# Kernel tuning notes

Measured on AMD Instinct MI355X. Metric: run time of the kernel, lower is better.

The kernel has to match this reference:

```python
import jax, jax.numpy as jnp
import numpy as np

SLOT_DIM, EMB_DIM, HID, ACT_DIM, NUM_ACT = 256, 256, 1024, 128, 1024
EPS_SAMPLE = 1e-6
EPS_LN = 1e-5


def setup_inputs() -> dict:
    key = jax.random.key(0)
    ks = jax.random.split(key, 12)
    B, N, S = 128, 32, 12
    s = 0.02
    return {
        "slots": jax.random.normal(ks[0], (B, N, S, SLOT_DIM), jnp.float32),
        "noise": jax.random.normal(ks[1], (B, N - 1, S, ACT_DIM), jnp.float32),
        "W1": jax.random.normal(ks[2], (SLOT_DIM, HID), jnp.float32) * s,
        "b1": jnp.zeros((HID,), jnp.float32),
        "ln_g": jnp.ones((HID,), jnp.float32),
        "ln_b": jnp.zeros((HID,), jnp.float32),
        "W2": jax.random.normal(ks[3], (HID, EMB_DIM), jnp.float32) * s,
        "b2": jnp.zeros((EMB_DIM,), jnp.float32),
        "Wm": jax.random.normal(ks[4], (EMB_DIM, ACT_DIM), jnp.float32) * s,
        "bm": jnp.zeros((ACT_DIM,), jnp.float32),
        "Wv": jax.random.normal(ks[5], (EMB_DIM, ACT_DIM), jnp.float32) * s,
        "bv": jnp.zeros((ACT_DIM,), jnp.float32),
        "codebook": jax.random.normal(ks[6], (NUM_ACT, ACT_DIM), jnp.float32) * s,
    }


def reference(slots, noise, W1, b1, ln_g, ln_b, W2, b2, Wm, bm, Wv, bv, codebook):
    sg = jax.lax.stop_gradient
    B, N, S, _ = slots.shape
    # per-slot MLP encoder: Linear -> ReLU -> LayerNorm -> Linear
    h = jax.nn.relu(jnp.einsum('bnsd,dh->bnsh', slots, W1) + b1)
    mu = h.mean(-1, keepdims=True)
    var = h.var(-1, keepdims=True)
    h = (h - mu) * jax.lax.rsqrt(var + EPS_LN) * ln_g + ln_b
    e = jnp.einsum('bnsh,he->bnse', h, W2) + b2  # (B,N,S,emb)
    # action distribution from consecutive frames
    mean_tok = jnp.einsum('bnse,ea->bnsa', e, Wm) + bm
    var_tok = jnp.abs(jnp.einsum('bnse,ea->bnsa', e, Wv) + bv)
    adm = mean_tok[:, 1:] - mean_tok[:, :-1]  # (B,N-1,S,A)
    adv = var_tok[:, 1:] + var_tok[:, :-1]
    action_dist = jnp.stack([adm, adv], axis=2)  # (B,N-1,2,S,A)
    # reparameterized sample
    z = noise * jnp.sqrt(adv + EPS_SAMPLE) + adm
    # VQ: nearest codebook entry via squared L2 distances
    zf = z.reshape(-1, ACT_DIM)  # (M,A)
    d = (jnp.sum(zf * zf, axis=1, keepdims=True)
         - 2.0 * zf @ codebook.T
         + jnp.sum(codebook * codebook, axis=1))  # (M,num_actions)
    idx = jnp.argmin(d, axis=1)  # (M,)
    q = codebook[idx].reshape(z.shape)
    quant_loss = jnp.mean((sg(z) - q) ** 2)
    commit_loss = jnp.mean((z - sg(q)) ** 2)
    q_st = z + sg(q - z)  # straight-through action prototypes
    action_variability = z - sg(q)
    action_idxs = idx.reshape(B, N - 1, S, 1)
    return (action_dist, z, action_variability, q_st, action_idxs, quant_loss, commit_loss)
```

## Files before the change

### kernel.cpp

```cpp
#include <hip/hip_runtime.h>
#include <math.h>

#define R_ROWS 49152
#define HID 1024
#define SLOT 256
#define EMB 256
#define ACT 128
#define NCODE 1024
#define M_ROWS 47616

#define OFF_AD 0
#define OFF_Z  12189696
#define OFF_AV 18284544
#define OFF_QS 24379392
#define OFF_IDX 30474240
#define OFF_QL 30521856
#define OFF_CL 30521857

#define WS_MT    0
#define WS_VT    6291456
#define WS_W1H  12582912
#define WS_W1L  12713984
#define WS_W2H  12845056
#define WS_W2L  12976128
#define WS_WMH  13107200
#define WS_WML  13123584
#define WS_WVH  13139968
#define WS_WVL  13156352
#define WS_CBH  13172736
#define WS_CBL  13238272
#define WS_CN   13303808
#define WS_LOSS 13304832

typedef _Float16 f16x8 __attribute__((ext_vector_type(8)));
typedef float f32x4 __attribute__((ext_vector_type(4)));
typedef float f32x16 __attribute__((ext_vector_type(16)));

__device__ __forceinline__ void pack_body(
    const float* __restrict__ W, _Float16* __restrict__ hi, _Float16* __restrict__ lo,
    int lgS, int N, int p)
{
    int j = p & 7;
    int l = (p >> 3) & 63;
    int q = p >> 9;
    int s = q & ((1 << lgS) - 1);
    int t = q >> lgS;
    int n = t * 16 + (l & 15);
    int k = s * 32 + ((l >> 4) << 3) + j;
    float x = W[(size_t)k * N + n];
    _Float16 h = (_Float16)x;
    hi[p] = h;
    lo[p] = (_Float16)(x - (float)h);
}

__global__ __launch_bounds__(256) void k_packall(
    const float* __restrict__ W1, const float* __restrict__ W2,
    const float* __restrict__ Wm, const float* __restrict__ Wv,
    const float* __restrict__ CB,
    _Float16* __restrict__ W1h, _Float16* __restrict__ W1l,
    _Float16* __restrict__ W2h, _Float16* __restrict__ W2l,
    _Float16* __restrict__ Wmh, _Float16* __restrict__ Wml,
    _Float16* __restrict__ Wvh, _Float16* __restrict__ Wvl,
    _Float16* __restrict__ CBh, _Float16* __restrict__ CBl,
    float* __restrict__ cn, float* __restrict__ losss)
{
    const int bi = blockIdx.x;
    const int tid = threadIdx.x;
    if (bi == 0 && tid == 0) *losss = 0.f;

    if (bi < 1024) {
        pack_body(W1, W1h, W1l, 3, HID, bi * 256 + tid);
    } else if (bi < 2048) {
        pack_body(W2, W2h, W2l, 5, EMB, (bi - 1024) * 256 + tid);
    } else if (bi < 2176) {
        pack_body(Wm, Wmh, Wml, 3, ACT, (bi - 2048) * 256 + tid);
    } else if (bi < 2304) {
        pack_body(Wv, Wvh, Wvl, 3, ACT, (bi - 2176) * 256 + tid);
    } else if (bi < 2816) {
        int p = (bi - 2304) * 256 + tid;
        int j = p & 7;
        int l = (p >> 3) & 63;
        int q = p >> 9;
        int s = q & 7;
        int t = q >> 3;
        int n = t * 32 + (l & 31);
        int k = s * 16 + ((l >> 5) << 3) + j;
        float x = CB[(size_t)n * ACT + k];
        _Float16 h = (_Float16)x;
        CBh[p] = h;
        CBl[p] = (_Float16)(x - (float)h);
    } else {
        int c = (bi - 2816) * 256 + tid;
        float s = 0.f;
        #pragma unroll
        for (int k = 0; k < ACT; k += 4) {
            float4 v = *(const float4*)&CB[(size_t)c * ACT + k];
            s += v.x*v.x + v.y*v.y + v.z*v.z + v.w*v.w;
        }
        cn[c] = s;
    }
}

__global__ __launch_bounds__(512, 4) void k_encoder_mfma(
    const float* __restrict__ X,
    const float* __restrict__ b1, const float* __restrict__ ln_g, const float* __restrict__ ln_b,
    const float* __restrict__ b2, const float* __restrict__ bm, const float* __restrict__ bv,
    const _Float16* __restrict__ W1h, const _Float16* __restrict__ W1l,
    const _Float16* __restrict__ W2h, const _Float16* __restrict__ W2l,
    const _Float16* __restrict__ Wmh, const _Float16* __restrict__ Wml,
    const _Float16* __restrict__ Wvh, const _Float16* __restrict__ Wvl,
    float* __restrict__ MT, float* __restrict__ VT)
{
    __shared__ _Float16 Hh0[16][1024];
    __shared__ _Float16 Hh1[16][1024];

    const int tid = threadIdx.x;
    const int w  = tid >> 6;
    const int l  = tid & 63;
    const int lr = l & 15;
    const int lg = l >> 4;
    const long rowbase = (long)blockIdx.x * 16;

    f16x8 a0[8], a1[8];
    {
        const float* xrow = X + (rowbase + lr) * SLOT + lg * 8;
        #pragma unroll
        for (int s = 0; s < 8; ++s) {
            float4 xa = *(const float4*)(xrow + 32 * s);
            float4 xb = *(const float4*)(xrow + 32 * s + 4);
            float xv[8] = {xa.x, xa.y, xa.z, xa.w, xb.x, xb.y, xb.z, xb.w};
            #pragma unroll
            for (int e = 0; e < 8; ++e) {
                _Float16 h = (_Float16)xv[e];
                a0[s][e] = h;
                a1[s][e] = (_Float16)(xv[e] - (float)h);
            }
        }
    }

    f32x4 acc[8];
    #pragma unroll
    for (int t = 0; t < 8; ++t) acc[t] = (f32x4){0.f, 0.f, 0.f, 0.f};

    #pragma unroll
    for (int s = 0; s < 8; ++s) {
        #pragma unroll
        for (int t = 0; t < 8; ++t) {
            int tg = w * 8 + t;
            f16x8 bh = *(const f16x8*)(W1h + ((size_t)(tg * 8 + s) * 64 + l) * 8);
            f16x8 bl = *(const f16x8*)(W1l + ((size_t)(tg * 8 + s) * 64 + l) * 8);
            acc[t] = __builtin_amdgcn_mfma_f32_16x16x32_f16(a0[s], bh, acc[t], 0, 0, 0);
            acc[t] = __builtin_amdgcn_mfma_f32_16x16x32_f16(a0[s], bl, acc[t], 0, 0, 0);
            acc[t] = __builtin_amdgcn_mfma_f32_16x16x32_f16(a1[s], bh, acc[t], 0, 0, 0);
        }
    }

    #pragma unroll
    for (int t = 0; t < 8; ++t) {
        float bb = b1[w * 128 + t * 16 + lr];
        #pragma unroll
        for (int r = 0; r < 4; ++r) acc[t][r] = fmaxf(acc[t][r] + bb, 0.f);
    }

    float sum[4] = {0,0,0,0}, sq[4] = {0,0,0,0};
    #pragma unroll
    for (int t = 0; t < 8; ++t)
        #pragma unroll
        for (int r = 0; r < 4; ++r) {
            float v = acc[t][r];
            sum[r] += v; sq[r] = fmaf(v, v, sq[r]);
        }
    #pragma unroll
    for (int off = 1; off < 16; off <<= 1)
        #pragma unroll
        for (int r = 0; r < 4; ++r) {
            sum[r] += __shfl_xor(sum[r], off, 64);
            sq[r]  += __shfl_xor(sq[r],  off, 64);
        }
    float* stat = (float*)&Hh0[0][0];
    if (lr == 0) {
        #pragma unroll
        for (int r = 0; r < 4; ++r) {
            stat[w * 16 + 4 * lg + r]       = sum[r];
            stat[128 + w * 16 + 4 * lg + r] = sq[r];
        }
    }
    __syncthreads();
    float mu[4], rs[4];
    #pragma unroll
    for (int r = 0; r < 4; ++r) {
        int m = 4 * lg + r;
        float s = 0.f, q = 0.f;
        #pragma unroll
        for (int wv = 0; wv < 8; ++wv) {
            s += stat[wv * 16 + m];
            q += stat[128 + wv * 16 + m];
        }
        float mmu = s * (1.f / HID);
        float var = q * (1.f / HID) - mmu * mmu;
        mu[r] = mmu;
        rs[r] = 1.f / sqrtf(var + 1e-5f);
    }
    __syncthreads();

    #pragma unroll
    for (int t = 0; t < 8; ++t) {
        int n = w * 128 + t * 16 + lr;
        float g = ln_g[n], be = ln_b[n];
        #pragma unroll
        for (int r = 0; r < 4; ++r) {
            int m = 4 * lg + r;
            float v = (acc[t][r] - mu[r]) * rs[r] * g + be;
            _Float16 h = (_Float16)v;
            _Float16 lo = (_Float16)(v - (float)h);
            int c = n >> 3, jj = n & 7;
            int cs = c ^ (m & 7);
            Hh0[m][cs * 8 + jj] = h;
            Hh1[m][cs * 8 + jj] = lo;
        }
    }
    __syncthreads();

    f32x4 acc2[2];
    #pragma unroll
    for (int t = 0; t < 2; ++t) acc2[t] = (f32x4){0.f, 0.f, 0.f, 0.f};

    #pragma unroll 4
    for (int s = 0; s < 32; ++s) {
        int cs = (4 * s + lg) ^ (lr & 7);
        f16x8 ah = *(const f16x8*)&Hh0[lr][cs * 8];
        f16x8 al = *(const f16x8*)&Hh1[lr][cs * 8];
        #pragma unroll
        for (int t = 0; t < 2; ++t) {
            int tg = w * 2 + t;
            f16x8 bh = *(const f16x8*)(W2h + ((size_t)(tg * 32 + s) * 64 + l) * 8);
            f16x8 bl = *(const f16x8*)(W2l + ((size_t)(tg * 32 + s) * 64 + l) * 8);
            acc2[t] = __builtin_amdgcn_mfma_f32_16x16x32_f16(ah, bh, acc2[t], 0, 0, 0);
            acc2[t] = __builtin_amdgcn_mfma_f32_16x16x32_f16(ah, bl, acc2[t], 0, 0, 0);
            acc2[t] = __builtin_amdgcn_mfma_f32_16x16x32_f16(al, bh, acc2[t], 0, 0, 0);
        }
    }
    __syncthreads();

    _Float16* Es0 = &Hh0[0][0];
    _Float16* Es1 = &Hh0[0][0] + 4096;
    #pragma unroll
    for (int t = 0; t < 2; ++t) {
        int n = w * 32 + t * 16 + lr;
        float bb2 = b2[n];
        #pragma unroll
        for (int r = 0; r < 4; ++r) {
            int m = 4 * lg + r;
            float v = acc2[t][r] + bb2;
            _Float16 h = (_Float16)v;
            _Float16 lo = (_Float16)(v - (float)h);
            int c = n >> 3, jj = n & 7;
            int cs = c ^ (m & 7);
            Es0[m * 256 + cs * 8 + jj] = h;
            Es1[m * 256 + cs * 8 + jj] = lo;
        }
    }
    __syncthreads();

    const _Float16* WXh = (w < 4) ? Wmh : Wvh;
    const _Float16* WXl = (w < 4) ? Wml : Wvl;
    f32x4 acc3[2];
    #pragma unroll
    for (int t = 0; t < 2; ++t) acc3[t] = (f32x4){0.f, 0.f, 0.f, 0.f};

    #pragma unroll
    for (int s = 0; s < 8; ++s) {
        int cs = (4 * s + lg) ^ (lr & 7);
        f16x8 ah = *(const f16x8*)&Es0[lr * 256 + cs * 8];
        f16x8 al = *(const f16x8*)&Es1[lr * 256 + cs * 8];
        #pragma unroll
        for (int t = 0; t < 2; ++t) {
            int tg = (w & 3) * 2 + t;
            f16x8 bh = *(const f16x8*)(WXh + ((size_t)(tg * 8 + s) * 64 + l) * 8);
            f16x8 bl = *(const f16x8*)(WXl + ((size_t)(tg * 8 + s) * 64 + l) * 8);
            acc3[t] = __builtin_amdgcn_mfma_f32_16x16x32_f16(ah, bh, acc3[t], 0, 0, 0);
            acc3[t] = __builtin_amdgcn_mfma_f32_16x16x32_f16(ah, bl, acc3[t], 0, 0, 0);
            acc3[t] = __builtin_amdgcn_mfma_f32_16x16x32_f16(al, bh, acc3[t], 0, 0, 0);
        }
    }

    #pragma unroll
    for (int t = 0; t < 2; ++t) {
        int a = (w & 3) * 32 + t * 16 + lr;
        float bx = (w < 4) ? bm[a] : bv[a];
        #pragma unroll
        for (int r = 0; r < 4; ++r) {
            float v = acc3[t][r] + bx;
            size_t row = rowbase + 4 * lg + r;
            if (w < 4) MT[row * ACT + a] = v;
            else       VT[row * ACT + a] = fabsf(v);
        }
    }
}

__global__ __launch_bounds__(256, 2) void k_vqfused(
    const float* __restrict__ MT, const float* __restrict__ VT,
    const float* __restrict__ noise,
    const _Float16* __restrict__ CBh, const _Float16* __restrict__ CBl,
    const float* __restrict__ cn, const float* __restrict__ CB,
    float* __restrict__ out, float* __restrict__ losss)
{
    __shared__ float4 Zs4[4096];
    __shared__ int   idx_s[128];
    __shared__ float red[4];
    float* Zs = (float*)Zs4;

    const int tid = threadIdx.x;
    const int rowbase = blockIdx.x * 128;
    const int a = tid & 127;
    const int rhalf = tid >> 7;

    #pragma unroll 8
    for (int i = 0; i < 64; ++i) {
        int row = 2 * i + rhalf;
        int m = rowbase + row;
        int b = m / 372;
        int r1 = m + 12 * b;
        int r2 = r1 + 12;
        float m1 = MT[(size_t)r1 * ACT + a], m2 = MT[(size_t)r2 * ACT + a];
        float v1 = VT[(size_t)r1 * ACT + a], v2 = VT[(size_t)r2 * ACT + a];
        float adm = m2 - m1;
        float adv = v2 + v1;
        float z = noise[(size_t)m * ACT + a] * sqrtf(adv + 1e-6f) + adm;
        int np = m / 12, s = m - np * 12;
        out[OFF_AD + (size_t)(np * 24 + s) * ACT + a] = adm;
        out[OFF_AD + (size_t)(np * 24 + 12 + s) * ACT + a] = adv;
        out[OFF_Z + (size_t)m * ACT + a] = z;
        Zs[row * 128 + (((a >> 2) ^ (row & 31)) << 2) + (a & 3)] = z;
    }
    __syncthreads();

    const int w = tid >> 6, l = tid & 63;
    const int col = l & 31, hw = l >> 5;
    const int arow = 32 * w + col;

    f16x8 a0[8], a1[8];
    #pragma unroll
    for (int s = 0; s < 8; ++s) {
        #pragma unroll
        for (int half = 0; half < 2; ++half) {
            int k4 = s * 4 + hw * 2 + half;
            float4 v = *(const float4*)&Zs[arow * 128 + ((k4 ^ (arow & 31)) << 2)];
            float xv[4] = {v.x, v.y, v.z, v.w};
            #pragma unroll
            for (int e = 0; e < 4; ++e) {
                _Float16 h = (_Float16)xv[e];
                a0[s][half * 4 + e] = h;
                a1[s][half * 4 + e] = (_Float16)(xv[e] - (float)h);
            }
        }
    }

    float best[16];
    int bidx[16];
    #pragma unroll
    for (int r = 0; r < 16; ++r) { best[r] = 3.4e38f; bidx[r] = 0; }

    for (int cb = 0; cb < 4; ++cb) {
        f32x16 acc[8];
        #pragma unroll
        for (int t = 0; t < 8; ++t)
            #pragma unroll
            for (int r = 0; r < 16; ++r) acc[t][r] = 0.f;

        #pragma unroll
        for (int s = 0; s < 8; ++s) {
            #pragma unroll
            for (int t = 0; t < 8; ++t) {
                int tg = cb * 8 + t;
                f16x8 bh = *(const f16x8*)(CBh + ((size_t)(tg * 8 + s) * 64 + l) * 8);
                f16x8 bl = *(const f16x8*)(CBl + ((size_t)(tg * 8 + s) * 64 + l) * 8);
                acc[t] = __builtin_amdgcn_mfma_f32_32x32x16_f16(a0[s], bh, acc[t], 0, 0, 0);
                acc[t] = __builtin_amdgcn_mfma_f32_32x32x16_f16(a0[s], bl, acc[t], 0, 0, 0);
                acc[t] = __builtin_amdgcn_mfma_f32_32x32x16_f16(a1[s], bh, acc[t], 0, 0, 0);
            }
        }

        float cnv[8];
        #pragma unroll
        for (int t = 0; t < 8; ++t) cnv[t] = cn[cb * 256 + t * 32 + col];

        #pragma unroll
        for (int reg = 0; reg < 16; ++reg) {
            #pragma unroll
            for (int t = 0; t < 8; ++t) {
                float d = cnv[t] - 2.f * acc[t][reg];
                int gi = cb * 256 + t * 32 + col;
                if (d < best[reg]) { best[reg] = d; bidx[reg] = gi; }
            }
        }
    }

    #pragma unroll
    for (int reg = 0; reg < 16; ++reg) {
        float bv_ = best[reg];
        int bi_ = bidx[reg];
        #pragma unroll
        for (int off = 1; off < 32; off <<= 1) {
            float ov = __shfl_xor(bv_, off, 64);
            int   oi = __shfl_xor(bi_, off, 64);
            if (ov < bv_ || (ov == bv_ && oi < bi_)) { bv_ = ov; bi_ = oi; }
        }
        if (col == 0) {
            int mloc = 32 * w + (reg & 3) + 8 * (reg >> 2) + 4 * hw;
            idx_s[mloc] = bi_;
            out[OFF_IDX + rowbase + mloc] = (float)bi_;
        }
    }
    __syncthreads();

    float ls = 0.f;
    #pragma unroll 8
    for (int i = 0; i < 64; ++i) {
        int row = 2 * i + rhalf;
        float z = Zs[row * 128 + (((a >> 2) ^ (row & 31)) << 2) + (a & 3)];
        int ci = idx_s[row];
        float q = CB[(size_t)ci * ACT + a];
        float diff = z - q;
        size_t m = (size_t)(rowbase + row);
        out[OFF_QS + m * ACT + a] = z + (q - z);
        out[OFF_AV + m * ACT + a] = diff;
        ls = fmaf(diff, diff, ls);
    }
    #pragma unroll
    for (int off = 32; off; off >>= 1) ls += __shfl_xor(ls, off, 64);
    if (l == 0) red[w] = ls;
    __syncthreads();
    if (tid == 0) atomicAdd(losss, red[0] + red[1] + red[2] + red[3]);
}

__global__ void k_losses(const float* __restrict__ losss, float* __restrict__ out)
{
    float v = *losss * (1.f / 6094848.f);
    out[OFF_QL] = v;
    out[OFF_CL] = v;
}

extern "C" void kernel_launch(void* const* d_in, const int* in_sizes, int n_in,
                              void* d_out, int out_size, void* d_ws, size_t ws_size,
                              hipStream_t stream)
{
    const float* slots = (const float*)d_in[0];
    const float* noise = (const float*)d_in[1];
    const float* W1    = (const float*)d_in[2];
    const float* b1    = (const float*)d_in[3];
    const float* ln_g  = (const float*)d_in[4];
    const float* ln_b  = (const float*)d_in[5];
    const float* W2    = (const float*)d_in[6];
    const float* b2    = (const float*)d_in[7];
    const float* Wm    = (const float*)d_in[8];
    const float* bm    = (const float*)d_in[9];
    const float* Wv    = (const float*)d_in[10];
    const float* bv    = (const float*)d_in[11];
    const float* CB    = (const float*)d_in[12];
    float* out = (float*)d_out;
    float* ws  = (float*)d_ws;

    float* MT   = ws + WS_MT;
    float* VT   = ws + WS_VT;
    float* cn   = ws + WS_CN;
    float* losss = ws + WS_LOSS;

    _Float16* W1h = (_Float16*)(ws + WS_W1H);
    _Float16* W1l = (_Float16*)(ws + WS_W1L);
    _Float16* W2h = (_Float16*)(ws + WS_W2H);
    _Float16* W2l = (_Float16*)(ws + WS_W2L);
    _Float16* Wmh = (_Float16*)(ws + WS_WMH);
    _Float16* Wml = (_Float16*)(ws + WS_WML);
    _Float16* Wvh = (_Float16*)(ws + WS_WVH);
    _Float16* Wvl = (_Float16*)(ws + WS_WVL);
    _Float16* CBh = (_Float16*)(ws + WS_CBH);
    _Float16* CBl = (_Float16*)(ws + WS_CBL);

    hipLaunchKernelGGL(k_packall, dim3(2820), dim3(256), 0, stream,
                       W1, W2, Wm, Wv, CB,
                       W1h, W1l, W2h, W2l, Wmh, Wml, Wvh, Wvl, CBh, CBl, cn, losss);
    hipLaunchKernelGGL(k_encoder_mfma, dim3(R_ROWS/16), dim3(512), 0, stream,
                       slots, b1, ln_g, ln_b, b2, bm, bv,
                       W1h, W1l, W2h, W2l, Wmh, Wml, Wvh, Wvl, MT, VT);
    hipLaunchKernelGGL(k_vqfused, dim3(M_ROWS/128), dim3(256), 0, stream,
                       MT, VT, noise, CBh, CBl, cn, CB, out, losss);
    hipLaunchKernelGGL(k_losses, dim3(1), dim3(1), 0, stream, losss, out);
}
```

Before: 447.4 us.

## Split encoder into tiled GEMM1/GEMM2 kernels with folded LayerNorm affine

Replaces the single fused encoder kernel, in which each 16-row block reloaded all of W1 and W2 from global memory, with two kernels. The first stages a 64-column slice of W1 in LDS and computes 128 rows per block, writing ReLU activations as fp16 hi/lo pairs plus per-slice LayerNorm partial sums to workspace. The second tiles 64 rows per block for the W2 and Wm/Wv GEMMs, and applies LayerNorm after the matmul by folding ln_g into W2 and precomputing ln_b·W2 + b2 and ln_g·W2 vectors. Rows are processed in two chunks so the intermediate buffer fits. This improves weight reuse but adds a global round trip for the hidden activations and more kernel launches, and the post-matmul normalisation may change rounding behaviour.

```diff
diff --git a/kernel.cpp b/kernel.cpp
--- a/kernel.cpp
+++ b/kernel.cpp
@@ -1,13 +1,14 @@
 #include <hip/hip_runtime.h>
 #include <math.h>
 
-#define R_ROWS 49152
 #define HID 1024
 #define SLOT 256
 #define EMB 256
 #define ACT 128
 #define NCODE 1024
+#define R_ROWS 49152
 #define M_ROWS 47616
+#define CH_ROWS 24576
 
 #define OFF_AD 0
 #define OFF_Z  12189696
@@ -30,15 +31,19 @@
 #define WS_CBH  13172736
 #define WS_CBL  13238272
 #define WS_CN   13303808
-#define WS_LOSS 13304832
+#define WS_V0   13304832
+#define WS_V1   13305088
+#define WS_LOSS 13305344
+#define WS_STATS 13305600
+#define WS_HH   14092032
+#define WS_HL   26674944
 
 typedef _Float16 f16x8 __attribute__((ext_vector_type(8)));
 typedef float f32x4 __attribute__((ext_vector_type(4)));
-typedef float f32x16 __attribute__((ext_vector_type(16)));
 
 __device__ __forceinline__ void pack_body(
     const float* __restrict__ W, _Float16* __restrict__ hi, _Float16* __restrict__ lo,
-    int lgS, int N, int p)
+    int lgS, int N, int p, const float* __restrict__ scale)
 {
     int j = p & 7;
     int l = (p >> 3) & 63;
@@ -48,6 +53,7 @@
     int n = t * 16 + (l & 15);
     int k = s * 32 + ((l >> 4) << 3) + j;
     float x = W[(size_t)k * N + n];
+    if (scale) x *= scale[k];
     _Float16 h = (_Float16)x;
     hi[p] = h;
     lo[p] = (_Float16)(x - (float)h);
@@ -56,26 +62,28 @@
 __global__ __launch_bounds__(256) void k_packall(
     const float* __restrict__ W1, const float* __restrict__ W2,
     const float* __restrict__ Wm, const float* __restrict__ Wv,
-    const float* __restrict__ CB,
+    const float* __restrict__ CB, const float* __restrict__ ln_g,
+    const float* __restrict__ ln_b, const float* __restrict__ b2,
     _Float16* __restrict__ W1h, _Float16* __restrict__ W1l,
     _Float16* __restrict__ W2h, _Float16* __restrict__ W2l,
     _Float16* __restrict__ Wmh, _Float16* __restrict__ Wml,
     _Float16* __restrict__ Wvh, _Float16* __restrict__ Wvl,
     _Float16* __restrict__ CBh, _Float16* __restrict__ CBl,
-    float* __restrict__ cn, float* __restrict__ losss)
+    float* __restrict__ cn, float* __restrict__ v0, float* __restrict__ v1,
+    float* __restrict__ losss)
 {
     const int bi = blockIdx.x;
     const int tid = threadIdx.x;
     if (bi == 0 && tid == 0) *losss = 0.f;
 
     if (bi < 1024) {
-        pack_body(W1, W1h, W1l, 3, HID, bi * 256 + tid);
+        pack_body(W1, W1h, W1l, 3, HID, bi * 256 + tid, (const float*)0);
     } else if (bi < 2048) {
-        pack_body(W2, W2h, W2l, 5, EMB, (bi - 1024) * 256 + tid);
+        pack_body(W2, W2h, W2l, 5, EMB, (bi - 1024) * 256 + tid, ln_g);
     } else if (bi < 2176) {
-        pack_body(Wm, Wmh, Wml, 3, ACT, (bi - 2048) * 256 + tid);
+        pack_body(Wm, Wmh, Wml, 3, ACT, (bi - 2048) * 256 + tid, (const float*)0);
     } else if (bi < 2304) {
-        pack_body(Wv, Wvh, Wvl, 3, ACT, (bi - 2176) * 256 + tid);
+        pack_body(Wv, Wvh, Wvl, 3, ACT, (bi - 2176) * 256 + tid, (const float*)0);
     } else if (bi < 2816) {
         int p = (bi - 2304) * 256 + tid;
         int j = p & 7;
@@ -89,7 +97,7 @@
         _Float16 h = (_Float16)x;
         CBh[p] = h;
         CBl[p] = (_Float16)(x - (float)h);
-    } else {
+    } else if (bi < 2820) {
         int c = (bi - 2816) * 256 + tid;
         float s = 0.f;
         #pragma unroll
@@ -98,32 +106,47 @@
             s += v.x*v.x + v.y*v.y + v.z*v.z + v.w*v.w;
         }
         cn[c] = s;
+    } else {
+        int n = tid;
+        float a0 = 0.f, a1 = 0.f;
+        for (int c = 0; c < HID; ++c) {
+            float w2 = W2[(size_t)c * EMB + n];
+            a1 = fmaf(ln_g[c], w2, a1);
+            a0 = fmaf(ln_b[c], w2, a0);
+        }
+        v1[n] = a1;
+        v0[n] = a0 + b2[n];
     }
 }
 
-__global__ __launch_bounds__(512, 4) void k_encoder_mfma(
-    const float* __restrict__ X,
-    const float* __restrict__ b1, const float* __restrict__ ln_g, const float* __restrict__ ln_b,
-    const float* __restrict__ b2, const float* __restrict__ bm, const float* __restrict__ bv,
+__global__ __launch_bounds__(512, 4) void k_gemm1(
+    const float* __restrict__ X, const float* __restrict__ b1,
     const _Float16* __restrict__ W1h, const _Float16* __restrict__ W1l,
-    const _Float16* __restrict__ W2h, const _Float16* __restrict__ W2l,
-    const _Float16* __restrict__ Wmh, const _Float16* __restrict__ Wml,
-    const _Float16* __restrict__ Wvh, const _Float16* __restrict__ Wvl,
-    float* __restrict__ MT, float* __restrict__ VT)
+    _Float16* __restrict__ GHh, _Float16* __restrict__ GHl,
+    float* __restrict__ stats, int row0)
 {
-    __shared__ _Float16 Hh0[16][1024];
-    __shared__ _Float16 Hh1[16][1024];
+    __shared__ _Float16 sh[32768];
 
     const int tid = threadIdx.x;
-    const int w  = tid >> 6;
-    const int l  = tid & 63;
-    const int lr = l & 15;
-    const int lg = l >> 4;
-    const long rowbase = (long)blockIdx.x * 16;
+    const int w = tid >> 6, l = tid & 63, lr = l & 15, lg = l >> 4;
+    const int p = blockIdx.x & 15;
+    const int rg = blockIdx.x >> 4;
+    const int rowc = rg * 128;
+
+    {
+        const float4* s0 = (const float4*)(W1h + (size_t)p * 16384);
+        const float4* s1 = (const float4*)(W1l + (size_t)p * 16384);
+        float4* d = (float4*)sh;
+        #pragma unroll
+        for (int i = 0; i < 4; ++i) {
+            d[tid + 512 * i] = s0[tid + 512 * i];
+            d[2048 + tid + 512 * i] = s1[tid + 512 * i];
+        }
+    }
 
     f16x8 a0[8], a1[8];
     {
-        const float* xrow = X + (rowbase + lr) * SLOT + lg * 8;
+        const float* xrow = X + (size_t)(row0 + rowc + w * 16 + lr) * SLOT + lg * 8;
         #pragma unroll
         for (int s = 0; s < 8; ++s) {
             float4 xa = *(const float4*)(xrow + 32 * s);
@@ -137,18 +160,18 @@
             }
         }
     }
-
-    f32x4 acc[8];
-    #pragma unroll
-    for (int t = 0; t < 8; ++t) acc[t] = (f32x4){0.f, 0.f, 0.f, 0.f};
+    __syncthreads();
+
+    f32x4 acc[4];
+    #pragma unroll
+    for (int t = 0; t < 4; ++t) acc[t] = (f32x4){0.f, 0.f, 0.f, 0.f};
 
     #pragma unroll
     for (int s = 0; s < 8; ++s) {
         #pragma unroll
-        for (int t = 0; t < 8; ++t) {
-            int tg = w * 8 + t;
-            f16x8 bh = *(const f16x8*)(W1h + ((size_t)(tg * 8 + s) * 64 + l) * 8);
-            f16x8 bl = *(const f16x8*)(W1l + ((size_t)(tg * 8 + s) * 64 + l) * 8);
+        for (int t = 0; t < 4; ++t) {
+            f16x8 bh = *(const f16x8*)&sh[((t * 8 + s) * 64 + l) * 8];
+            f16x8 bl = *(const f16x8*)&sh[16384 + ((t * 8 + s) * 64 + l) * 8];
             acc[t] = __builtin_amdgcn_mfma_f32_16x16x32_f16(a0[s], bh, acc[t], 0, 0, 0);
             acc[t] = __builtin_amdgcn_mfma_f32_16x16x32_f16(a0[s], bl, acc[t], 0, 0, 0);
             acc[t] = __builtin_amdgcn_mfma_f32_16x16x32_f16(a1[s], bh, acc[t], 0, 0, 0);
@@ -156,144 +179,225 @@
     }
 
     #pragma unroll
-    for (int t = 0; t < 8; ++t) {
-        float bb = b1[w * 128 + t * 16 + lr];
+    for (int t = 0; t < 4; ++t) {
+        float bb = b1[p * 64 + t * 16 + lr];
         #pragma unroll
         for (int r = 0; r < 4; ++r) acc[t][r] = fmaxf(acc[t][r] + bb, 0.f);
     }
 
-    float sum[4] = {0,0,0,0}, sq[4] = {0,0,0,0};
-    #pragma unroll
-    for (int t = 0; t < 8; ++t)
+    {
+        float sum[4] = {0,0,0,0}, sq[4] = {0,0,0,0};
+        #pragma unroll
+        for (int t = 0; t < 4; ++t)
+            #pragma unroll
+            for (int r = 0; r < 4; ++r) {
+                float v = acc[t][r];
+                sum[r] += v; sq[r] = fmaf(v, v, sq[r]);
+            }
+        #pragma unroll
+        for (int off = 1; off < 16; off <<= 1)
+            #pragma unroll
+            for (int r = 0; r < 4; ++r) {
+                sum[r] += __shfl_xor(sum[r], off, 64);
+                sq[r]  += __shfl_xor(sq[r],  off, 64);
+            }
+        if (lr == 0) {
+            #pragma unroll
+            for (int r = 0; r < 4; ++r) {
+                size_t row = (size_t)rowc + w * 16 + lg * 4 + r;
+                float2 st = {sum[r], sq[r]};
+                *(float2*)&stats[((size_t)p * CH_ROWS + row) * 2] = st;
+            }
+        }
+    }
+    __syncthreads();
+
+    #pragma unroll
+    for (int t = 0; t < 4; ++t) {
         #pragma unroll
         for (int r = 0; r < 4; ++r) {
+            int rowloc = w * 16 + lg * 4 + r;
+            int col = t * 16 + lr;
+            int cc = col >> 3, j = col & 7;
+            int ad = rowloc * 64 + ((cc ^ (rowloc & 7)) << 3) + j;
             float v = acc[t][r];
-            sum[r] += v; sq[r] = fmaf(v, v, sq[r]);
-        }
-    #pragma unroll
-    for (int off = 1; off < 16; off <<= 1)
-        #pragma unroll
-        for (int r = 0; r < 4; ++r) {
-            sum[r] += __shfl_xor(sum[r], off, 64);
-            sq[r]  += __shfl_xor(sq[r],  off, 64);
-        }
-    float* stat = (float*)&Hh0[0][0];
-    if (lr == 0) {
-        #pragma unroll
-        for (int r = 0; r < 4; ++r) {
-            stat[w * 16 + 4 * lg + r]       = sum[r];
-            stat[128 + w * 16 + 4 * lg + r] = sq[r];
-        }
-    }
-    __syncthreads();
-    float mu[4], rs[4];
-    #pragma unroll
-    for (int r = 0; r < 4; ++r) {
-        int m = 4 * lg + r;
+            _Float16 h = (_Float16)v;
+            sh[ad] = h;
+            sh[8192 + ad] = (_Float16)(v - (float)h);
+        }
+    }
+    __syncthreads();
+
+    #pragma unroll
+    for (int i = 0; i < 2; ++i) {
+        int u = tid + 512 * i;
+        int RTl = u >> 7;
+        int Sl  = (u >> 6) & 1;
+        int li  = u & 63;
+        int row = RTl * 16 + (li & 15);
+        int cc  = Sl * 4 + (li >> 4);
+        int ad  = row * 64 + ((cc ^ (row & 7)) << 3);
+        f16x8 vh = *(const f16x8*)&sh[ad];
+        f16x8 vl = *(const f16x8*)&sh[8192 + ad];
+        size_t RTg = (size_t)rg * 8 + RTl;
+        size_t off = ((RTg * 32 + (2 * p + Sl)) * 64 + li) * 8;
+        *(f16x8*)&GHh[off] = vh;
+        *(f16x8*)&GHl[off] = vl;
+    }
+}
+
+__global__ __launch_bounds__(512, 4) void k_gemm2(
+    const _Float16* __restrict__ GHh, const _Float16* __restrict__ GHl,
+    const _Float16* __restrict__ W2h, const _Float16* __restrict__ W2l,
+    const _Float16* __restrict__ Wmh, const _Float16* __restrict__ Wml,
+    const _Float16* __restrict__ Wvh, const _Float16* __restrict__ Wvl,
+    const float* __restrict__ stats, const float* __restrict__ v0,
+    const float* __restrict__ v1, const float* __restrict__ bm,
+    const float* __restrict__ bv,
+    float* __restrict__ MT, float* __restrict__ VT, int row0)
+{
+    __shared__ _Float16 sh[32768];
+    __shared__ float mu_s[64], rs_s[64];
+
+    const int tid = threadIdx.x;
+    const int w = tid >> 6, l = tid & 63, lr = l & 15, lg = l >> 4;
+    const int rb = blockIdx.x;
+    const int rowc0 = rb * 64;
+
+    if (tid < 64) {
         float s = 0.f, q = 0.f;
         #pragma unroll
-        for (int wv = 0; wv < 8; ++wv) {
-            s += stat[wv * 16 + m];
-            q += stat[128 + wv * 16 + m];
-        }
-        float mmu = s * (1.f / HID);
-        float var = q * (1.f / HID) - mmu * mmu;
-        mu[r] = mmu;
-        rs[r] = 1.f / sqrtf(var + 1e-5f);
-    }
-    __syncthreads();
-
-    #pragma unroll
-    for (int t = 0; t < 8; ++t) {
-        int n = w * 128 + t * 16 + lr;
-        float g = ln_g[n], be = ln_b[n];
-        #pragma unroll
-        for (int r = 0; r < 4; ++r) {
-            int m = 4 * lg + r;
-            float v = (acc[t][r] - mu[r]) * rs[r] * g + be;
-            _Float16 h = (_Float16)v;
-            _Float16 lo = (_Float16)(v - (float)h);
-            int c = n >> 3, jj = n & 7;
-            int cs = c ^ (m & 7);
-            Hh0[m][cs * 8 + jj] = h;
-            Hh1[m][cs * 8 + jj] = lo;
-        }
-    }
-    __syncthreads();
-
-    f32x4 acc2[2];
-    #pragma unroll
-    for (int t = 0; t < 2; ++t) acc2[t] = (f32x4){0.f, 0.f, 0.f, 0.f};
-
-    #pragma unroll 4
-    for (int s = 0; s < 32; ++s) {
-        int cs = (4 * s + lg) ^ (lr & 7);
-        f16x8 ah = *(const f16x8*)&Hh0[lr][cs * 8];
-        f16x8 al = *(const f16x8*)&Hh1[lr][cs * 8];
-        #pragma unroll
-        for (int t = 0; t < 2; ++t) {
-            int tg = w * 2 + t;
-            f16x8 bh = *(const f16x8*)(W2h + ((size_t)(tg * 32 + s) * 64 + l) * 8);
-            f16x8 bl = *(const f16x8*)(W2l + ((size_t)(tg * 32 + s) * 64 + l) * 8);
-            acc2[t] = __builtin_amdgcn_mfma_f32_16x16x32_f16(ah, bh, acc2[t], 0, 0, 0);
-            acc2[t] = __builtin_amdgcn_mfma_f32_16x16x32_f16(ah, bl, acc2[t], 0, 0, 0);
-            acc2[t] = __builtin_amdgcn_mfma_f32_16x16x32_f16(al, bh, acc2[t], 0, 0, 0);
-        }
-    }
-    __syncthreads();
-
-    _Float16* Es0 = &Hh0[0][0];
-    _Float16* Es1 = &Hh0[0][0] + 4096;
+        for (int pp = 0; pp < 16; ++pp) {
+            float2 st = *(const float2*)&stats[((size_t)pp * CH_ROWS + rowc0 + tid) * 2];
+            s += st.x; q += st.y;
+        }
+        float mu = s * (1.f / HID);
+        float var = q * (1.f / HID) - mu * mu;
+        mu_s[tid] = mu;
+        rs_s[tid] = 1.f / sqrtf(var + 1e-5f);
+    }
+
+    float v0r[2], v1r[2];
     #pragma unroll
     for (int t = 0; t < 2; ++t) {
         int n = w * 32 + t * 16 + lr;
-        float bb2 = b2[n];
-        #pragma unroll
-        for (int r = 0; r < 4; ++r) {
-            int m = 4 * lg + r;
-            float v = acc2[t][r] + bb2;
-            _Float16 h = (_Float16)v;
-            _Float16 lo = (_Float16)(v - (float)h);
-            int c = n >> 3, jj = n & 7;
-            int cs = c ^ (m & 7);
-            Es0[m * 256 + cs * 8 + jj] = h;
-            Es1[m * 256 + cs * 8 + jj] = lo;
+        v0r[t] = v0[n];
+        v1r[t] = v1[n];
+    }
+
+    f32x4 acc[4][2];
+    #pragma unroll
+    for (int rt = 0; rt < 4; ++rt)
+        #pragma unroll
+        for (int t = 0; t < 2; ++t) acc[rt][t] = (f32x4){0.f, 0.f, 0.f, 0.f};
+
+    for (int kp = 0; kp < 8; ++kp) {
+        __syncthreads();
+        #pragma unroll
+        for (int i = 0; i < 4; ++i) {
+            int u = tid + 512 * i;
+            int arr = u >> 10;
+            int ui = u & 1023;
+            int RTl = ui >> 8;
+            int rem = ui & 255;
+            size_t gu = ((size_t)(rb * 4 + RTl) * 32 + kp * 4) * 64 + rem;
+            const _Float16* src = arr ? GHl : GHh;
+            *(f16x8*)&sh[(size_t)arr * 8192 + (size_t)ui * 8] = *(const f16x8*)&src[gu * 8];
+        }
+        __syncthreads();
+
+        #pragma unroll
+        for (int sl = 0; sl < 4; ++sl) {
+            f16x8 bh[2], bl[2];
+            #pragma unroll
+            for (int t = 0; t < 2; ++t) {
+                int tg = w * 2 + t;
+                size_t o = ((size_t)(tg * 32 + kp * 4 + sl) * 64 + l) * 8;
+                bh[t] = *(const f16x8*)&W2h[o];
+                bl[t] = *(const f16x8*)&W2l[o];
+            }
+            #pragma unroll
+            for (int rt = 0; rt < 4; ++rt) {
+                f16x8 ah = *(const f16x8*)&sh[((rt * 4 + sl) * 64 + l) * 8];
+                f16x8 al = *(const f16x8*)&sh[8192 + ((rt * 4 + sl) * 64 + l) * 8];
+                #pragma unroll
+                for (int t = 0; t < 2; ++t) {
+                    acc[rt][t] = __builtin_amdgcn_mfma_f32_16x16x32_f16(ah, bh[t], acc[rt][t], 0, 0, 0);
+                    acc[rt][t] = __builtin_amdgcn_mfma_f32_16x16x32_f16(ah, bl[t], acc[rt][t], 0, 0, 0);
+                    acc[rt][t] = __builtin_amdgcn_mfma_f32_16x16x32_f16(al, bh[t], acc[rt][t], 0, 0, 0);
+                }
+            }
+        }
+    }
+    __syncthreads();
+
+    #pragma unroll
+    for (int rt = 0; rt < 4; ++rt) {
+        #pragma unroll
+        for (int t = 0; t < 2; ++t) {
+            int n = w * 32 + t * 16 + lr;
+            int cc = n >> 3, j = n & 7;
+            #pragma unroll
+            for (int r = 0; r < 4; ++r) {
+                int row = rt * 16 + lg * 4 + r;
+                float mu = mu_s[row], rs = rs_s[row];
+                float e = rs * acc[rt][t][r] - rs * mu * v1r[t] + v0r[t];
+                _Float16 h = (_Float16)e;
+                int ad = row * 256 + ((cc ^ (row & 7)) << 3) + j;
+                sh[ad] = h;
+                sh[16384 + ad] = (_Float16)(e - (float)h);
+            }
         }
     }
     __syncthreads();
 
     const _Float16* WXh = (w < 4) ? Wmh : Wvh;
     const _Float16* WXl = (w < 4) ? Wml : Wvl;
-    f32x4 acc3[2];
-    #pragma unroll
-    for (int t = 0; t < 2; ++t) acc3[t] = (f32x4){0.f, 0.f, 0.f, 0.f};
+    f32x4 acc3[4][2];
+    #pragma unroll
+    for (int rt = 0; rt < 4; ++rt)
+        #pragma unroll
+        for (int t = 0; t < 2; ++t) acc3[rt][t] = (f32x4){0.f, 0.f, 0.f, 0.f};
 
     #pragma unroll
     for (int s = 0; s < 8; ++s) {
-        int cs = (4 * s + lg) ^ (lr & 7);
-        f16x8 ah = *(const f16x8*)&Es0[lr * 256 + cs * 8];
-        f16x8 al = *(const f16x8*)&Es1[lr * 256 + cs * 8];
+        f16x8 bh[2], bl[2];
         #pragma unroll
         for (int t = 0; t < 2; ++t) {
             int tg = (w & 3) * 2 + t;
-            f16x8 bh = *(const f16x8*)(WXh + ((size_t)(tg * 8 + s) * 64 + l) * 8);
-            f16x8 bl = *(const f16x8*)(WXl + ((size_t)(tg * 8 + s) * 64 + l) * 8);
-            acc3[t] = __builtin_amdgcn_mfma_f32_16x16x32_f16(ah, bh, acc3[t], 0, 0, 0);
-            acc3[t] = __builtin_amdgcn_mfma_f32_16x16x32_f16(ah, bl, acc3[t], 0, 0, 0);
-            acc3[t] = __builtin_amdgcn_mfma_f32_16x16x32_f16(al, bh, acc3[t], 0, 0, 0);
-        }
-    }
-
-    #pragma unroll
-    for (int t = 0; t < 2; ++t) {
-        int a = (w & 3) * 32 + t * 16 + lr;
-        float bx = (w < 4) ? bm[a] : bv[a];
-        #pragma unroll
-        for (int r = 0; r < 4; ++r) {
-            float v = acc3[t][r] + bx;
-            size_t row = rowbase + 4 * lg + r;
-            if (w < 4) MT[row * ACT + a] = v;
-            else       VT[row * ACT + a] = fabsf(v);
+            size_t o = ((size_t)(tg * 8 + s) * 64 + l) * 8;
+            bh[t] = *(const f16x8*)&WXh[o];
+            bl[t] = *(const f16x8*)&WXl[o];
+        }
+        #pragma unroll
+        for (int rt = 0; rt < 4; ++rt) {
+            int row = rt * 16 + lr;
+            int cc = s * 4 + lg;
+            int ad = row * 256 + ((cc ^ (row & 7)) << 3);
+            f16x8 ah = *(const f16x8*)&sh[ad];
+            f16x8 al = *(const f16x8*)&sh[16384 + ad];
+            #pragma unroll
+            for (int t = 0; t < 2; ++t) {
+                acc3[rt][t] = __builtin_amdgcn_mfma_f32_16x16x32_f16(ah, bh[t], acc3[rt][t], 0, 0, 0);
+                acc3[rt][t] = __builtin_amdgcn_mfma_f32_16x16x32_f16(ah, bl[t], acc3[rt][t], 0, 0, 0);
+                acc3[rt][t] = __builtin_amdgcn_mfma_f32_16x16x32_f16(al, bh[t], acc3[rt][t], 0, 0, 0);
+            }
+        }
+    }
+
+    #pragma unroll
+    for (int rt = 0; rt < 4; ++rt) {
+        #pragma unroll
+        for (int t = 0; t < 2; ++t) {
+            int a = (w & 3) * 32 + t * 16 + lr;
+            float bx = (w < 4) ? bm[a] : bv[a];
+            #pragma unroll
+            for (int r = 0; r < 4; ++r) {
+                size_t grow = (size_t)row0 + rowc0 + rt * 16 + lg * 4 + r;
+                float vv = acc3[rt][t][r] + bx;
+                if (w < 4) MT[grow * ACT + a] = vv;
+                else       VT[grow * ACT + a] = fabsf(vv);
+            }
         }
     }
 }
@@ -305,6 +409,7 @@
     const float* __restrict__ cn, const float* __restrict__ CB,
     float* __restrict__ out, float* __restrict__ losss)
 {
+    typedef float f32x16 __attribute__((ext_vector_type(16)));
     __shared__ float4 Zs4[4096];
     __shared__ int   idx_s[128];
     __shared__ float red[4];
@@ -461,10 +566,13 @@
     float* out = (float*)d_out;
     float* ws  = (float*)d_ws;
 
-    float* MT   = ws + WS_MT;
-    float* VT   = ws + WS_VT;
-    float* cn   = ws + WS_CN;
+    float* MT    = ws + WS_MT;
+    float* VT    = ws + WS_VT;
+    float* cn    = ws + WS_CN;
+    float* v0    = ws + WS_V0;
+    float* v1    = ws + WS_V1;
     float* losss = ws + WS_LOSS;
+    float* stats = ws + WS_STATS;
 
     _Float16* W1h = (_Float16*)(ws + WS_W1H);
     _Float16* W1l = (_Float16*)(ws + WS_W1L);
@@ -476,14 +584,24 @@
     _Float16* Wvl = (_Float16*)(ws + WS_WVL);
     _Float16* CBh = (_Float16*)(ws + WS_CBH);
     _Float16* CBl = (_Float16*)(ws + WS_CBL);
-
-    hipLaunchKernelGGL(k_packall, dim3(2820), dim3(256), 0, stream,
-                       W1, W2, Wm, Wv, CB,
-                       W1h, W1l, W2h, W2l, Wmh, Wml, Wvh, Wvl, CBh, CBl, cn, losss);
-    hipLaunchKernelGGL(k_encoder_mfma, dim3(R_ROWS/16), dim3(512), 0, stream,
-                       slots, b1, ln_g, ln_b, b2, bm, bv,
-                       W1h, W1l, W2h, W2l, Wmh, Wml, Wvh, Wvl, MT, VT);
-    hipLaunchKernelGGL(k_vqfused, dim3(M_ROWS/128), dim3(256), 0, stream,
+    _Float16* GHh = (_Float16*)(ws + WS_HH);
+    _Float16* GHl = (_Float16*)(ws + WS_HL);
+
+    hipLaunchKernelGGL(k_packall, dim3(2821), dim3(256), 0, stream,
+                       W1, W2, Wm, Wv, CB, ln_g, ln_b, b2,
+                       W1h, W1l, W2h, W2l, Wmh, Wml, Wvh, Wvl, CBh, CBl,
+                       cn, v0, v1, losss);
+
+    for (int c = 0; c < 2; ++c) {
+        int row0 = c * CH_ROWS;
+        hipLaunchKernelGGL(k_gemm1, dim3((CH_ROWS / 128) * 16), dim3(512), 0, stream,
+                           slots, b1, W1h, W1l, GHh, GHl, stats, row0);
+        hipLaunchKernelGGL(k_gemm2, dim3(CH_ROWS / 64), dim3(512), 0, stream,
+                           GHh, GHl, W2h, W2l, Wmh, Wml, Wvh, Wvl,
+                           stats, v0, v1, bm, bv, MT, VT, row0);
+    }
+
+    hipLaunchKernelGGL(k_vqfused, dim3(M_ROWS / 128), dim3(256), 0, stream,
                        MT, VT, noise, CBh, CBl, cn, CB, out, losss);
     hipLaunchKernelGGL(k_losses, dim3(1), dim3(1), 0, stream, losss, out);
 }
```

After: 532.0 us. 18.9% more time.
